# Performance work log

Hardware: AMD Instinct MI355X
Metric: run time of the kernel (lower is better)

## Reference

```python
import jax, jax.numpy as jnp
import numpy as np

# Constants from the module's __init__ (LIFNodes / RUMNodes / Connection args)
DT = 1.0
TAU = 10.0            # LIF membrane time constant
TC_TRACE = 20.0       # spike-trace time constant (bindsnet default)
REST, RESET, THRESH = -70.0, -65.0, -55.0
ALPHA, BETA = 0.95, 0.8     # RUM hidden leak / threshold-adaptation decay
H_THRESH = 1.0              # hidden firing threshold
NU1_PRE, NU1_POST = 0.001, 0.01    # PostPre STDP rates (input->hidden)
NU2 = 0.0001                        # MSTDP learning rate (hidden->output)
WMIN, WMAX = 0.0, 1.0
REWARD = 1.0
A_PLUS, A_MINUS = 1.0, -1.0         # MSTDP trace amplitudes (bindsnet defaults)
TC_PM = 20.0                        # MSTDP p_plus/p_minus time constant
INPUT_GAIN = 20.0   # scales U[0,1) rates into the LIF operating range (rest->thresh gap = 15 mV)

IN_D, HID_D, OUT_D = 544, 1024, 2048


def setup_inputs() -> dict:
    key = jax.random.key(0)
    k1, k2, k3 = jax.random.split(key, 3)
    x = jax.random.uniform(k1, (IN_D,), dtype=jnp.float32)            # rate-coded input
    w1 = jax.random.uniform(k2, (IN_D, HID_D), dtype=jnp.float32)     # in [wmin, wmax]
    w2 = jax.random.uniform(k3, (HID_D, OUT_D), dtype=jnp.float32)
    return {"x": x, "w1": w1, "w2": w2, "num_timesteps": 500}


def _simulate(x, w1, w2, T):
    decay_v = jnp.float32(np.exp(-DT / TAU))
    decay_tr = jnp.float32(np.exp(-DT / TC_TRACE))
    decay_pm = jnp.float32(np.exp(-DT / TC_PM))
    rates = x * INPUT_GAIN  # constant input current each timestep (rate coding)

    carry = (
        jnp.full((IN_D,), REST, jnp.float32),   # v_in
        jnp.zeros((HID_D,), jnp.float32),        # v_hid
        jnp.full((OUT_D,), REST, jnp.float32),   # v_out
        jnp.zeros((IN_D,), jnp.float32),         # tr_in  (pre trace, PostPre)
        jnp.zeros((HID_D,), jnp.float32),        # tr_hid (post trace, PostPre)
        jnp.zeros((HID_D,), jnp.float32),        # b_hid  (RUM threshold adaptation)
        jnp.zeros((HID_D,), jnp.float32),        # p_plus  (MSTDP pre trace)
        jnp.zeros((OUT_D,), jnp.float32),        # p_minus (MSTDP post trace)
        w1, w2,
    )

    def step(c, _):
        v_in, v_hid, v_out, tr_in, tr_hid, b_hid, p_plus, p_minus, w1c, w2c = c
        # --- input LIF: decay toward rest, integrate rates, spike, reset ---
        v_in = decay_v * (v_in - REST) + REST + rates
        s_in = (v_in >= THRESH).astype(jnp.float32)
        v_in = jnp.where(s_in > 0, RESET, v_in)
        tr_in = jnp.where(s_in > 0, 1.0, tr_in * decay_tr)
        # --- hidden RUM: leaky integration (alpha) + adaptive threshold (beta) ---
        i_hid = s_in @ w1c                                  # [HID]
        v_hid = ALPHA * v_hid + i_hid
        s_hid = (v_hid >= H_THRESH + b_hid).astype(jnp.float32)
        v_hid = jnp.where(s_hid > 0, 0.0, v_hid)
        b_hid = BETA * b_hid + s_hid
        tr_hid_new = jnp.where(s_hid > 0, 1.0, tr_hid * decay_tr)
        # --- output LIF ---
        i_out = s_hid @ w2c                                 # [OUT]
        v_out = decay_v * (v_out - REST) + REST + i_out
        s_out = (v_out >= THRESH).astype(jnp.float32)
        v_out = jnp.where(s_out > 0, RESET, v_out)
        # --- PostPre STDP on w1: potentiate on post spike, depress on pre spike ---
        w1c = jnp.clip(
            w1c + NU1_POST * jnp.outer(tr_in, s_hid) - NU1_PRE * jnp.outer(s_in, tr_hid_new),
            WMIN, WMAX)
        # --- MSTDP on w2: reward-modulated eligibility ---
        p_plus = decay_pm * p_plus + A_PLUS * s_hid
        p_minus = decay_pm * p_minus + A_MINUS * s_out
        elig = jnp.outer(p_plus, s_out) + jnp.outer(s_hid, p_minus)  # [HID, OUT]
        w2c = w2c + NU2 * REWARD * DT * elig
        new_c = (v_in, v_hid, v_out, tr_in, tr_hid_new, b_hid, p_plus, p_minus, w1c, w2c)
        return new_c, s_out

    _, spikes = jax.lax.scan(step, carry, None, length=T)
    return spikes  # [T, OUT_D] float32 spike raster (== stacked monitor recording)


def reference(x, w1, w2, num_timesteps):
    return _simulate(x, w1, w2, num_timesteps)
```

## Files before the change

kernel.cpp:

```cpp
#include <hip/hip_runtime.h>
#include <stdint.h>


#define DECAY_V  0.90483741803595952f
#define DECAY_TR 0.95122942450071403f
#define REST_F   (-70.0f)
#define RESET_F  (-65.0f)
#define THRESH_F (-55.0f)
#define ALPHA_F  (0.95f)
#define BETA_F   (0.8f)
#define NU1_PRE_F  (0.001f)
#define NU1_POST_F (0.01f)
#define NU2_F      (0.0001f)
#define GAIN_F     (20.0f)
#define LOG2D    (-0.072134752044448170f)

static constexpr int IN_D  = 544;
static constexpr int HID_D = 1024;
static constexpr int OUT_D = 2048;
static constexpr int TMAX  = 512;

#define DP1  0.95122942450071403f
#define DP2  0.90483741803595957f
#define DP4  0.81873075307798186f
#define DP8  0.67032004603563930f
#define DP16 0.44932896411722159f
#define DP32 0.20189651799465541f

__device__ __forceinline__ float rdlane(float x, int l) {
    return __builtin_bit_cast(float,
        __builtin_amdgcn_readlane(__builtin_bit_cast(int, x), l));
}

template <int CTRL>
__device__ __forceinline__ float dpp_add(float x) {
    int y = __builtin_amdgcn_update_dpp(0, __builtin_bit_cast(int, x),
                                        CTRL, 0xF, 0xF, true);
    return x + __builtin_bit_cast(float, y);
}

__device__ __forceinline__ float wave_sum64(float x) {
    x = dpp_add<0xB1>(x);
    x = dpp_add<0x4E>(x);
    x = dpp_add<0x114>(x);
    x = dpp_add<0x118>(x);
    x = dpp_add<0x142>(x);
    x = dpp_add<0x143>(x);
    return rdlane(x, 63);
}

__global__ __launch_bounds__(256, 2)
void hidden_kernel(const float* __restrict__ x, const float* __restrict__ w1,
                   const int* __restrict__ Tp, float* __restrict__ Sf)
{
    const int T = Tp[0];
    const int tid = threadIdx.x, lane = tid & 63, wv = tid >> 6;
    const int cp = wv >> 1;
    const int h  = wv & 1;
    const int col = blockIdx.x * 2 + cp;
    const float c0 = REST_F * (1.0f - DECAY_V);
    __shared__ float part[2][4];

    float w[5], vi[5], tr[5], cadd[5];
    #pragma unroll
    for (int k = 0; k < 5; ++k) {
        const int o = 64 * k + lane;
        const int i = 272 * h + o;
        const bool ok = (o < 272);
        w[k]    = ok ? w1[(size_t)i * HID_D + col] : 0.f;
        cadd[k] = c0 + (ok ? x[i] * GAIN_F : 0.f);
        vi[k]   = REST_F;
        tr[k]   = 0.f;
    }
    float v_h = 0.f, b_h = 0.f, tr_h = 0.f;

    for (int t = 0; t < T; ++t) {
        float acc = 0.f, s[5];
        #pragma unroll
        for (int k = 0; k < 5; ++k) {
            const float vv = fmaf(DECAY_V, vi[k], cadd[k]);
            const bool sp = (vv >= THRESH_F);
            vi[k] = sp ? RESET_F : vv;
            s[k]  = sp ? 1.f : 0.f;
            tr[k] = fmaxf(tr[k] * DECAY_TR, s[k]);
            acc   = fmaf(s[k], w[k], acc);
        }
        const float p = wave_sum64(acc);
        const int par = t & 1;
        if (lane == 0) part[par][wv] = p;
        __syncthreads();
        const float tot = p + part[par][wv ^ 1];
        const float vh2 = fmaf(ALPHA_F, v_h, tot);
        const bool hp = (vh2 >= 1.0f + b_h);
        const float sh = hp ? 1.f : 0.f;
        v_h  = hp ? 0.f : vh2;
        b_h  = fmaf(BETA_F, b_h, sh);
        tr_h = hp ? 1.f : tr_h * DECAY_TR;
        const float apot = hp ? NU1_POST_F : 0.f;
        const float adep = NU1_PRE_F * tr_h;
        #pragma unroll
        for (int k = 0; k < 5; ++k) {
            const float a  = fmaf(apot, tr[k], w[k]);
            const float nw = fmaf(-adep, s[k], a);
            w[k] = __builtin_amdgcn_fmed3f(nw, 0.f, 1.f);
        }
        if (h == 0 && lane == 0) Sf[(size_t)t * HID_D + col] = sh;
    }
}

__global__ void pack_kernel(float* __restrict__ Sf, const int* __restrict__ Tp,
                            unsigned long long* __restrict__ Sb)
{
    const int T = Tp[0];
    const int t = blockIdx.x;
    const int lane = threadIdx.x & 63, wv = threadIdx.x >> 6;
    if (t >= T) {
        ((float4*)(Sf + (size_t)t * HID_D))[threadIdx.x] = make_float4(0.f, 0.f, 0.f, 0.f);
        return;
    }
    #pragma unroll
    for (int q = 0; q < 4; ++q) {
        const int word = wv * 4 + q;
        const float s = Sf[(size_t)t * HID_D + word * 64 + lane];
        const unsigned long long m = __ballot(s > 0.5f);
        if (lane == 0) Sb[(size_t)t * 16 + word] = m;
    }
}

__global__ void gram_kernel(const unsigned long long* __restrict__ Sb,
                            const int* __restrict__ Tp, float* __restrict__ G)
{
    const int T = Tp[0];
    if ((int)blockIdx.x > (int)blockIdx.y) return;
    const int tid = threadIdx.x;
    __shared__ unsigned long long tR[16][17], uR[16][17];
    {
        const int r = tid >> 4, w = tid & 15;
        const int trow = blockIdx.y * 16 + r, urow = blockIdx.x * 16 + r;
        tR[r][w] = (trow < T) ? Sb[(size_t)trow * 16 + w] : 0ULL;
        uR[r][w] = (urow < T) ? Sb[(size_t)urow * 16 + w] : 0ULL;
    }
    __syncthreads();
    const int tx = tid & 15, ty = tid >> 4;
    const int t = blockIdx.y * 16 + ty, u = blockIdx.x * 16 + tx;
    if (t < T && u < t) {
        int s = 0;
        #pragma unroll
        for (int w = 0; w < 16; ++w) s += __popcll(tR[ty][w] & uR[tx][w]);
        G[(size_t)t * TMAX + u] = (float)s;
    }
}

__global__ __launch_bounds__(256)
void mt_kernel(const float* __restrict__ G, const int* __restrict__ Tp,
               float* __restrict__ MT)
{
    const int T = Tp[0];
    const int lane = threadIdx.x & 63;
    const int t = blockIdx.x * 4 + (threadIdx.x >> 6);
    if (t >= T) return;
    const float* Gr = G + (size_t)t * TMAX;
    const float dl1  = exp2f((float)(lane + 1) * LOG2D);
    const float d64l = exp2f((float)(64 - lane) * LOG2D);

    float g[8], kk[8];
    #pragma unroll
    for (int c = 0; c < 8; ++c) {
        const int tau = 64 * c + lane;
        g[c] = (tau < t) ? Gr[tau] : 0.f;
    }
    float kc = 0.f;
    #pragma unroll
    for (int c = 7; c >= 0; --c) {
        float k = g[c], u;
        u = __shfl_down(k, 1, 64);  if (lane < 63) k = fmaf(DP1, u, k);
        u = __shfl_down(k, 2, 64);  if (lane < 62) k = fmaf(DP2, u, k);
        u = __shfl_down(k, 4, 64);  if (lane < 60) k = fmaf(DP4, u, k);
        u = __shfl_down(k, 8, 64);  if (lane < 56) k = fmaf(DP8, u, k);
        u = __shfl_down(k, 16, 64); if (lane < 48) k = fmaf(DP16, u, k);
        u = __shfl_down(k, 32, 64); if (lane < 32) k = fmaf(DP32, u, k);
        k = fmaf(d64l, kc, k);
        kk[c] = k;
        kc = rdlane(k, 0);
    }
    float hc = 0.f;
    #pragma unroll
    for (int c = 0; c < 8; ++c) {
        float h = g[c], u;
        u = __shfl_up(h, 1, 64);  if (lane >= 1)  h = fmaf(DP1, u, h);
        u = __shfl_up(h, 2, 64);  if (lane >= 2)  h = fmaf(DP2, u, h);
        u = __shfl_up(h, 4, 64);  if (lane >= 4)  h = fmaf(DP4, u, h);
        u = __shfl_up(h, 8, 64);  if (lane >= 8)  h = fmaf(DP8, u, h);
        u = __shfl_up(h, 16, 64); if (lane >= 16) h = fmaf(DP16, u, h);
        u = __shfl_up(h, 32, 64); if (lane >= 32) h = fmaf(DP32, u, h);
        h = fmaf(dl1, hc, h);
        const int tau = 64 * c + lane;
        if (tau < t) MT[(size_t)tau * TMAX + t] = NU2_F * (h - kk[c]);
        hc = rdlane(h, 63);
    }
}

__global__ __launch_bounds__(256)
void gemm_kernel(const float* __restrict__ Sf, const float* __restrict__ w2,
                 float* __restrict__ AT, int klen)
{
    const int j0 = blockIdx.x * 128;
    const int t0 = blockIdx.y * 64;
    const int kbase = blockIdx.z * 512;
    float* ATp = AT + (size_t)blockIdx.z * OUT_D * TMAX;
    __shared__ float Ss[16][68];
    __shared__ float Ws[16][192];
    const int tid = threadIdx.x;
    const int sr = tid >> 2, sq = tid & 3;
    const int wq2 = tid & 31, wr2 = tid >> 5;
    const int wcol = (wq2 >> 1) * 12 + (wq2 & 1) * 4;
    const int tj = tid & 15, tt = tid >> 4;
    const int tjc = tj * 12;

    float acc[4][8];
    #pragma unroll
    for (int a = 0; a < 4; ++a)
        #pragma unroll
        for (int b = 0; b < 8; ++b) acc[a][b] = 0.f;

    for (int k0 = 0; k0 < klen; k0 += 16) {
        const float4 sv = *(const float4*)&Sf[(size_t)(t0 + sr) * HID_D + kbase + k0 + sq * 4];
        const float4 wa = *(const float4*)&w2[(size_t)(kbase + k0 + wr2) * OUT_D + j0 + wq2 * 4];
        const float4 wb = *(const float4*)&w2[(size_t)(kbase + k0 + wr2 + 8) * OUT_D + j0 + wq2 * 4];
        __syncthreads();
        Ss[sq * 4 + 0][sr] = sv.x;
        Ss[sq * 4 + 1][sr] = sv.y;
        Ss[sq * 4 + 2][sr] = sv.z;
        Ss[sq * 4 + 3][sr] = sv.w;
        *(float4*)&Ws[wr2][wcol] = wa;
        *(float4*)&Ws[wr2 + 8][wcol] = wb;
        __syncthreads();
        #pragma unroll
        for (int kk = 0; kk < 16; ++kk) {
            const float4 a4 = *(const float4*)&Ss[kk][tt * 4];
            const float4 b0 = *(const float4*)&Ws[kk][tjc];
            const float4 b1 = *(const float4*)&Ws[kk][tjc + 4];
            const float aa[4] = {a4.x, a4.y, a4.z, a4.w};
            const float bb[8] = {b0.x, b0.y, b0.z, b0.w, b1.x, b1.y, b1.z, b1.w};
            #pragma unroll
            for (int ti = 0; ti < 4; ++ti)
                #pragma unroll
                for (int jj = 0; jj < 8; ++jj)
                    acc[ti][jj] = fmaf(aa[ti], bb[jj], acc[ti][jj]);
        }
    }
    #pragma unroll
    for (int jj = 0; jj < 8; ++jj)
        *(float4*)&AT[(size_t)blockIdx.z * OUT_D * TMAX +
                      (size_t)(j0 + tj * 8 + jj) * TMAX + t0 + tt * 4] =
            make_float4(acc[0][jj], acc[1][jj], acc[2][jj], acc[3][jj]);
    (void)ATp;
}

template <int C>
__device__ __forceinline__ void out_chunk(
    const float* __restrict__ AT, const float* __restrict__ MT,
    float (&hsA)[8], float (&hsB)[8], float& vA, float& vB,
    float* __restrict__ out, int j, int lane, int T, int nparts,
    float* __restrict__ LD, float2* __restrict__ so2)
{
    const int rem = T - 64 * C;
    const int mtv = (rem < 64) ? rem : 64;
    float avA = AT[(size_t)j * TMAX + 64 * C + lane];
    float avB = AT[(size_t)(j + 1) * TMAX + 64 * C + lane];
    if (nparts == 2) {
        avA += AT[(size_t)(OUT_D + j) * TMAX + 64 * C + lane];
        avB += AT[(size_t)(OUT_D + j + 1) * TMAX + 64 * C + lane];
    }
    const float* ldb = LD + (C & 1) * 4096;
    float accA = hsA[C], accB = hsB[C];
    float mv0 = ldb[lane];
    float mv1 = (mtv > 1) ? ldb[64 + lane] : 0.f;
    for (int tt = 0; tt < mtv; ++tt) {
        const float mv = mv0;
        mv0 = mv1;
        if (tt + 2 < mtv) mv1 = ldb[(tt + 2) * 64 + lane];
        const float ivA = rdlane(avA + accA, tt);
        const float ivB = rdlane(avB + accB, tt);
        const float vdA = fmaf(DECAY_V, vA, REST_F * (1.0f - DECAY_V)) + ivA;
        const float vdB = fmaf(DECAY_V, vB, REST_F * (1.0f - DECAY_V)) + ivB;
        const bool spA = (vdA >= THRESH_F);
        const bool spB = (vdB >= THRESH_F);
        const float soA = spA ? 1.f : 0.f;
        const float soB = spB ? 1.f : 0.f;
        vA = spA ? RESET_F : vdA;
        vB = spB ? RESET_F : vdB;
        if (lane == 0)
            *(float2*)&out[(size_t)(64 * C + tt) * OUT_D + j] = make_float2(soA, soB);
        if (lane == tt) so2[tt] = make_float2(soA, soB);
        accA = fmaf(soA, mv, accA);
        accB = fmaf(soB, mv, accB);
    }
    if (C + 1 < 8 && 64 * (C + 1) < T) {
        {
            float* dst = LD + ((C + 1) & 1) * 4096;
            const float* src = MT + (size_t)(64 * (C + 1)) * TMAX + 64 * (C + 1) + lane;
            #pragma unroll 16
            for (int r = 0; r < 64; ++r) {
                const float v = src[(size_t)r * TMAX];
                dst[r * 64 + lane] = (r < lane) ? v : 0.f;
            }
        }
        for (int tt = 0; tt < mtv; ++tt) {
            const float2 s = so2[tt];
            const float* Mrow = MT + (size_t)(64 * C + tt) * TMAX + lane;
            #pragma unroll
            for (int K = C + 1; K < 8; ++K) {
                const float mval = Mrow[64 * K];
                hsA[K] = fmaf(s.x, mval, hsA[K]);
                hsB[K] = fmaf(s.y, mval, hsB[K]);
            }
        }
    }
}

__global__ __launch_bounds__(64, 2)
void out_kernel(const float* __restrict__ AT, const float* __restrict__ MT,
                const int* __restrict__ Tp, float* __restrict__ out, int nparts)
{
    const int T = Tp[0];
    const int lane = threadIdx.x;
    const int j = blockIdx.x * 2;
    __shared__ float LD[2 * 4096];
    __shared__ float2 so2[64];

    float hsA[8], hsB[8];
    #pragma unroll
    for (int k = 0; k < 8; ++k) { hsA[k] = 0.f; hsB[k] = 0.f; }
    float vA = REST_F, vB = REST_F;

    {
        const float* src = MT + lane;
        #pragma unroll 16
        for (int r = 0; r < 64; ++r) {
            const float v = src[(size_t)r * TMAX];
            LD[r * 64 + lane] = (r < lane) ? v : 0.f;
        }
    }
    out_chunk<0>(AT, MT, hsA, hsB, vA, vB, out, j, lane, T, nparts, LD, so2);
    if (T >  64) out_chunk<1>(AT, MT, hsA, hsB, vA, vB, out, j, lane, T, nparts, LD, so2);
    if (T > 128) out_chunk<2>(AT, MT, hsA, hsB, vA, vB, out, j, lane, T, nparts, LD, so2);
    if (T > 192) out_chunk<3>(AT, MT, hsA, hsB, vA, vB, out, j, lane, T, nparts, LD, so2);
    if (T > 256) out_chunk<4>(AT, MT, hsA, hsB, vA, vB, out, j, lane, T, nparts, LD, so2);
    if (T > 320) out_chunk<5>(AT, MT, hsA, hsB, vA, vB, out, j, lane, T, nparts, LD, so2);
    if (T > 384) out_chunk<6>(AT, MT, hsA, hsB, vA, vB, out, j, lane, T, nparts, LD, so2);
    if (T > 448) out_chunk<7>(AT, MT, hsA, hsB, vA, vB, out, j, lane, T, nparts, LD, so2);
}

extern "C" void kernel_launch(void* const* d_in, const int* in_sizes, int n_in,
                              void* d_out, int out_size, void* d_ws, size_t ws_size,
                              hipStream_t stream) {
    const float* x  = (const float*)d_in[0];
    const float* w1 = (const float*)d_in[1];
    const float* w2 = (const float*)d_in[2];
    const int*   Tp = (const int*)d_in[3];
    float* out = (float*)d_out;
    char* ws = (char*)d_ws;
    unsigned long long* Sb = (unsigned long long*)(ws);
    float* G  = (float*)(ws + 65536);
    float* MT = (float*)(ws + 65536 + 1048576);
    float* Sf = (float*)(ws + 65536 + 2 * 1048576);
    float* AT = (float*)(ws + 65536 + 4 * 1048576);
    const size_t need2 = 65536 + 4 * 1048576 + 2 * 4194304;
    const int nparts = (ws_size >= need2) ? 2 : 1;
    const int klen = (nparts == 2) ? 512 : 1024;

    hipLaunchKernelGGL(hidden_kernel, dim3(HID_D / 2), dim3(256), 0, stream, x, w1, Tp, Sf);
    hipLaunchKernelGGL(pack_kernel,   dim3(TMAX), dim3(256), 0, stream, Sf, Tp, Sb);
    hipLaunchKernelGGL(gram_kernel,   dim3(32, 32), dim3(256), 0, stream, Sb, Tp, G);
    hipLaunchKernelGGL(mt_kernel,     dim3(128), dim3(256), 0, stream, G, Tp, MT);
    hipLaunchKernelGGL(gemm_kernel,   dim3(16, 8, nparts), dim3(256), 0, stream,
                       Sf, w2, AT, klen);
    hipLaunchKernelGGL(out_kernel,    dim3(OUT_D / 2), dim3(64), 0, stream, AT, MT, Tp, out, nparts);
}
```

Measured before the change: 321.6 us.

## Precompute input-layer spike bitmasks in a separate kernel for hidden kernel

Adds a single-block input_kernel that simulates the input LIF layer once and writes per-timestep 64-bit spike ballots to workspace. The hidden kernel no longer recomputes the input neuron dynamics redundantly in every block; it loads and realigns the bitmasks (prefetching the next step) and converts bits to 0/1 with v_cndmask. This removes per-step redundant work from the serial hidden loop, at the cost of an extra serial launch of T steps and global loads each step.

Result: slower. 482.0 us (+49.9%).

```diff
diff --git a/kernel.cpp b/kernel.cpp
--- a/kernel.cpp
+++ b/kernel.cpp
@@ -49,39 +49,78 @@
     return rdlane(x, 63);
 }
 
+__device__ __forceinline__ float mask_sel(uint64_t m) {
+    float r;
+    asm("v_cndmask_b32 %0, 0, 1.0, %1" : "=v"(r) : "s"(m));
+    return r;
+}
+
+__global__ __launch_bounds__(576)
+void input_kernel(const float* __restrict__ x, const int* __restrict__ Tp,
+                  unsigned long long* __restrict__ Sm)
+{
+    const int T = Tp[0];
+    const int tid = threadIdx.x, lane = tid & 63, wv = tid >> 6;
+    const bool ok = (tid < IN_D);
+    for (int t = tid; t < T; t += 576) Sm[(size_t)t * 10 + 9] = 0ULL;
+    const float cadd = REST_F * (1.0f - DECAY_V) + (ok ? x[tid] * GAIN_F : -1000.0f);
+    float v = REST_F;
+    for (int t = 0; t < T; ++t) {
+        const float vv = fmaf(DECAY_V, v, cadd);
+        const bool sp = (vv >= THRESH_F);
+        const unsigned long long m = __ballot(sp);
+        v = sp ? RESET_F : vv;
+        if (lane == 0) Sm[(size_t)t * 10 + wv] = m;
+    }
+}
+
 __global__ __launch_bounds__(256, 2)
-void hidden_kernel(const float* __restrict__ x, const float* __restrict__ w1,
+void hidden_kernel(const unsigned long long* __restrict__ Sm,
+                   const float* __restrict__ w1,
                    const int* __restrict__ Tp, float* __restrict__ Sf)
 {
     const int T = Tp[0];
     const int tid = threadIdx.x, lane = tid & 63, wv = tid >> 6;
     const int cp = wv >> 1;
     const int h  = wv & 1;
+    const int hh = __builtin_amdgcn_readfirstlane(h);
     const int col = blockIdx.x * 2 + cp;
-    const float c0 = REST_F * (1.0f - DECAY_V);
     __shared__ float part[2][4];
 
-    float w[5], vi[5], tr[5], cadd[5];
+    float w[5], tr[5];
     #pragma unroll
     for (int k = 0; k < 5; ++k) {
         const int o = 64 * k + lane;
         const int i = 272 * h + o;
-        const bool ok = (o < 272);
-        w[k]    = ok ? w1[(size_t)i * HID_D + col] : 0.f;
-        cadd[k] = c0 + (ok ? x[i] * GAIN_F : 0.f);
-        vi[k]   = REST_F;
-        tr[k]   = 0.f;
+        w[k]  = (o < 272) ? w1[(size_t)i * HID_D + col] : 0.f;
+        tr[k] = 0.f;
     }
     float v_h = 0.f, b_h = 0.f, tr_h = 0.f;
 
+    uint64_t Mc[5], Mn[5];
+    auto ldm = [&](uint64_t (&M)[5], int t) {
+        const unsigned long long* __restrict__ p = Sm + (size_t)t * 10;
+        if (hh == 0) {
+            M[0] = p[0]; M[1] = p[1]; M[2] = p[2]; M[3] = p[3];
+            M[4] = p[4] & 0xFFFFull;
+        } else {
+            const uint64_t a = p[4], b = p[5], c = p[6], d = p[7],
+                           e = p[8], f = p[9];
+            M[0] = (a >> 16) | (b << 48);
+            M[1] = (b >> 16) | (c << 48);
+            M[2] = (c >> 16) | (d << 48);
+            M[3] = (d >> 16) | (e << 48);
+            M[4] = (e >> 16) | (f << 48);
+        }
+    };
+    ldm(Mc, 0);
+
     for (int t = 0; t < T; ++t) {
+        if (t + 1 < T) ldm(Mn, t + 1);
         float acc = 0.f, s[5];
         #pragma unroll
         for (int k = 0; k < 5; ++k) {
-            const float vv = fmaf(DECAY_V, vi[k], cadd[k]);
-            const bool sp = (vv >= THRESH_F);
-            vi[k] = sp ? RESET_F : vv;
-            s[k]  = sp ? 1.f : 0.f;
+            s[k]  = mask_sel(Mc[k]);
             tr[k] = fmaxf(tr[k] * DECAY_TR, s[k]);
             acc   = fmaf(s[k], w[k], acc);
         }
@@ -105,6 +144,8 @@
             w[k] = __builtin_amdgcn_fmed3f(nw, 0.f, 1.f);
         }
         if (h == 0 && lane == 0) Sf[(size_t)t * HID_D + col] = sh;
+        #pragma unroll
+        for (int k = 0; k < 5; ++k) Mc[k] = Mn[k];
     }
 }
 
@@ -207,7 +248,6 @@
     const int j0 = blockIdx.x * 128;
     const int t0 = blockIdx.y * 64;
     const int kbase = blockIdx.z * 512;
-    float* ATp = AT + (size_t)blockIdx.z * OUT_D * TMAX;
     __shared__ float Ss[16][68];
     __shared__ float Ws[16][192];
     const int tid = threadIdx.x;
@@ -254,7 +294,6 @@
         *(float4*)&AT[(size_t)blockIdx.z * OUT_D * TMAX +
                       (size_t)(j0 + tj * 8 + jj) * TMAX + t0 + tt * 4] =
             make_float4(acc[0][jj], acc[1][jj], acc[2][jj], acc[3][jj]);
-    (void)ATp;
 }
 
 template <int C>
@@ -361,16 +400,18 @@
     const int*   Tp = (const int*)d_in[3];
     float* out = (float*)d_out;
     char* ws = (char*)d_ws;
-    unsigned long long* Sb = (unsigned long long*)(ws);
-    float* G  = (float*)(ws + 65536);
-    float* MT = (float*)(ws + 65536 + 1048576);
-    float* Sf = (float*)(ws + 65536 + 2 * 1048576);
-    float* AT = (float*)(ws + 65536 + 4 * 1048576);
-    const size_t need2 = 65536 + 4 * 1048576 + 2 * 4194304;
+    unsigned long long* Sm = (unsigned long long*)(ws);
+    unsigned long long* Sb = (unsigned long long*)(ws + 65536);
+    float* G  = (float*)(ws + 131072);
+    float* MT = (float*)(ws + 131072 + 1048576);
+    float* Sf = (float*)(ws + 131072 + 2 * 1048576);
+    float* AT = (float*)(ws + 131072 + 4 * 1048576);
+    const size_t need2 = 131072 + 4 * 1048576 + 2 * 4194304;
     const int nparts = (ws_size >= need2) ? 2 : 1;
     const int klen = (nparts == 2) ? 512 : 1024;
 
-    hipLaunchKernelGGL(hidden_kernel, dim3(HID_D / 2), dim3(256), 0, stream, x, w1, Tp, Sf);
+    hipLaunchKernelGGL(input_kernel,  dim3(1), dim3(576), 0, stream, x, Tp, Sm);
+    hipLaunchKernelGGL(hidden_kernel, dim3(HID_D / 2), dim3(256), 0, stream, Sm, w1, Tp, Sf);
     hipLaunchKernelGGL(pack_kernel,   dim3(TMAX), dim3(256), 0, stream, Sf, Tp, Sb);
     hipLaunchKernelGGL(gram_kernel,   dim3(32, 32), dim3(256), 0, stream, Sb, Tp, G);
     hipLaunchKernelGGL(mt_kernel,     dim3(128), dim3(256), 0, stream, G, Tp, MT);
```
